# Kernel tuning notes

Measured on AMD Instinct MI355X. Metric: run time of the kernel, lower is better.

The kernel has to match this reference:

```python
import jax, jax.numpy as jnp
import numpy as np

B, IMG_DIM, H, W = 2, 256, 64, 64
PC_C, PC_D = 16, 16          # voxel_dim = PC_C * PC_D = 256
VOXEL_DIM = PC_C * PC_D
QK_DIM = 256                 # out_channels of img_conv / voxel_conv


def _conv1x1(x, w, b):
    # x: [B, Cin, H, W], w: [Cout, Cin], b: [Cout]  (1x1 conv == per-pixel matmul)
    return jnp.einsum('bchw,oc->bohw', x, w) + b[None, :, None, None]


def setup_inputs() -> dict:
    key = jax.random.key(0)
    ks = jax.random.split(key, 10)
    s = 0.02
    return {
        'img': jax.random.normal(ks[0], (B, IMG_DIM, H, W), jnp.float32),
        'pc': jax.random.normal(ks[1], (B, PC_D, H, W, PC_C), jnp.float32),  # dense() layout [B,D,H,W,C]
        'img_conv_w': jax.random.normal(ks[2], (QK_DIM, IMG_DIM), jnp.float32) * s,
        'img_conv_b': jnp.zeros((QK_DIM,), jnp.float32),
        'voxel_conv_w': jax.random.normal(ks[3], (QK_DIM, VOXEL_DIM), jnp.float32) * s,
        'voxel_conv_b': jnp.zeros((QK_DIM,), jnp.float32),
        'img_v_w': jax.random.normal(ks[4], (IMG_DIM, IMG_DIM), jnp.float32) * s,
        'img_v_b': jnp.zeros((IMG_DIM,), jnp.float32),
        'voxel_v_w': jax.random.normal(ks[5], (VOXEL_DIM, VOXEL_DIM), jnp.float32) * s,
        'voxel_v_b': jnp.zeros((VOXEL_DIM,), jnp.float32),
    }


def reference(img, pc, img_conv_w, img_conv_b, voxel_conv_w, voxel_conv_b,
              img_v_w, img_v_b, voxel_v_w, voxel_v_b):
    b, c_img, h, w = img.shape
    # pc.dense() -> permute(0,4,1,2,3) -> [B, C, D, H, W] -> [B, C*D, H, W]
    pc = jnp.transpose(pc, (0, 4, 1, 2, 3))
    pcb, pcc, pcd, pch, pcw = pc.shape
    pc2 = pc.reshape(pcb, pcc * pcd, pch, pcw)
    n = h * w  # == pch * pcw (required by the bmms)

    img_q = _conv1x1(img, img_conv_w, img_conv_b).reshape(b, QK_DIM, n).transpose(0, 2, 1)  # [B, N, 256]
    pc_k = _conv1x1(pc2, voxel_conv_w, voxel_conv_b).reshape(b, QK_DIM, n)                  # [B, 256, N]
    # unscaled single-head cross attention, softmax over voxel positions
    attn = jax.nn.softmax(jnp.einsum('bnc,bcm->bnm', img_q, pc_k), axis=-1)                 # [B, N_img, N_pc]

    img_v = _conv1x1(img, img_v_w, img_v_b).reshape(b, c_img, n)                            # [B, C_img, N]
    img_v = jnp.einsum('bcn,bmn->bcm', img_v, attn).reshape(b, c_img, h, w)                 # img_v @ attn^T

    pc_v = _conv1x1(pc2, voxel_v_w, voxel_v_b).reshape(b, pcc * pcd, n)                     # [B, C*D, N]
    pc_v = jnp.einsum('bcn,bmn->bcm', pc_v, attn).reshape(b, pcc, pcd, pch, pcw)
    return (img_v, pc_v)
```

## Files before the change

### kernel.cpp

```cpp
#include <hip/hip_runtime.h>
#include <hip/hip_bf16.h>


typedef __hip_bfloat16 bf16;
typedef __attribute__((ext_vector_type(8))) short bf16x8;
typedef __attribute__((ext_vector_type(4))) float f32x4;

#define AS1 __attribute__((address_space(1)))
#define AS3 __attribute__((address_space(3)))

__device__ __forceinline__ void gld_lds16(const bf16* g, bf16* s) {
    __builtin_amdgcn_global_load_lds((const AS1 void*)g, (AS3 void*)s, 16, 0, 0);
}

__global__ __launch_bounds__(256) void proj_kernel(
    const float* __restrict__ img, const float* __restrict__ pc,
    const float* __restrict__ Wq,  const float* __restrict__ bq,
    const float* __restrict__ Wk,  const float* __restrict__ bk,
    const float* __restrict__ Wvi, const float* __restrict__ bvi,
    const float* __restrict__ Wvp, const float* __restrict__ bvp,
    bf16* __restrict__ Qw, bf16* __restrict__ Ktw, bf16* __restrict__ Vall)
{
    __shared__ __align__(16) bf16 XT[64][264];
    __shared__ __align__(16) bf16 Wst[256 * 32];

    const int blk = blockIdx.x;
    const int s   = blk >> 8;
    const int b   = (blk >> 7) & 1;
    const int g   = (blk >> 6) & 1;
    const int n0  = (blk & 63) * 64;
    const int tid = threadIdx.x;

    if (s == 0) {
        const float* src = img + b * 1048576;
        for (int k = 0; k < 16; k++) {
            const int i = tid + k * 256;
            const int cin = i >> 4, nl4 = (i & 15) * 4;
            const float4 v = *(const float4*)&src[cin * 4096 + n0 + nl4];
            XT[nl4 + 0][cin] = __float2bfloat16(v.x);
            XT[nl4 + 1][cin] = __float2bfloat16(v.y);
            XT[nl4 + 2][cin] = __float2bfloat16(v.z);
            XT[nl4 + 3][cin] = __float2bfloat16(v.w);
        }
    } else {
        const float* src = pc + b * 1048576;
        for (int k = 0; k < 16; k++) {
            const int d = k, u = tid;
            const int nl = u >> 2, c4 = (u & 3) * 4;
            const float4 v = *(const float4*)&src[d * 65536 + (n0 + nl) * 16 + c4];
            XT[nl][(c4 + 0) * 16 + d] = __float2bfloat16(v.x);
            XT[nl][(c4 + 1) * 16 + d] = __float2bfloat16(v.y);
            XT[nl][(c4 + 2) * 16 + d] = __float2bfloat16(v.z);
            XT[nl][(c4 + 3) * 16 + d] = __float2bfloat16(v.w);
        }
    }

    const float* W = s ? (g ? Wvp : Wk) : (g ? Wvi : Wq);
    const float* Bv = s ? (g ? bvp : bk) : (g ? bvi : bq);

    const int wv = tid >> 6, lane = tid & 63, l16 = lane & 15, quad = lane >> 4;
    const int ob = wv * 64;

    f32x4 acc[4][4] = {};

    for (int ks = 0; ks < 8; ks++) {
        const int k0 = ks * 32;
        __syncthreads();
        for (int j = 0; j < 8; j++) {
            const int idx = j * 256 + tid;
            const int row = idx >> 3, c4 = (idx & 7) * 4;
            const float4 v = *(const float4*)&W[row * 256 + k0 + c4];
            bf16 t4[4];
            t4[0] = __float2bfloat16(v.x); t4[1] = __float2bfloat16(v.y);
            t4[2] = __float2bfloat16(v.z); t4[3] = __float2bfloat16(v.w);
            const int sl = (c4 >> 3) ^ ((row >> 1) & 3);
            *(uint2*)&Wst[row * 32 + sl * 8 + (c4 & 4)] = *(const uint2*)t4;
        }
        __syncthreads();

        bf16x8 af[4], wf[4];
        for (int ti = 0; ti < 4; ti++)
            af[ti] = *(const bf16x8*)&XT[ti * 16 + l16][k0 + quad * 8];
        for (int tj = 0; tj < 4; tj++) {
            const int rw = ob + tj * 16 + l16;
            wf[tj] = *(const bf16x8*)&Wst[rw * 32 + (quad ^ ((rw >> 1) & 3)) * 8];
        }
        for (int ti = 0; ti < 4; ti++)
            for (int tj = 0; tj < 4; tj++)
                acc[ti][tj] = __builtin_amdgcn_mfma_f32_16x16x32_bf16(af[ti], wf[tj], acc[ti][tj], 0, 0, 0);
    }

    if (g == 0) {
        bf16* D1 = (s ? Ktw : Qw) + b * (4096 * 256);
        for (int tj = 0; tj < 4; tj++) {
            const int o = ob + tj * 16 + l16;
            const float bias = Bv[o];
            for (int ti = 0; ti < 4; ti++) {
                const int nl = ti * 16 + quad * 4;
                for (int r = 0; r < 4; r++)
                    D1[(n0 + nl + r) * 256 + o] = __float2bfloat16(acc[ti][tj][r] + bias);
            }
        }
    } else {
        bf16* D2 = Vall + b * (512 * 4096) + (s ? 256 * 4096 : 0);
        for (int tj = 0; tj < 4; tj++) {
            const int o = ob + tj * 16 + l16;
            const float bias = Bv[o];
            for (int ti = 0; ti < 4; ti++) {
                const int nl = ti * 16 + quad * 4;
                bf16 pv[4];
                for (int r = 0; r < 4; r++)
                    pv[r] = __float2bfloat16(acc[ti][tj][r] + bias);
                *(uint2*)&D2[o * 4096 + n0 + nl] = *(const uint2*)pv;
            }
        }
    }
}

__global__ __launch_bounds__(256, 4) void attn_s_kernel(
    const bf16* __restrict__ Qw, const bf16* __restrict__ Ktw,
    bf16* __restrict__ Pt, float* __restrict__ Lpart)
{
    __shared__ __align__(16) bf16 smem[2][8192];

    const int b  = blockIdx.z;
    const int q0 = blockIdx.y * 128;
    const int p0 = blockIdx.x * 128;
    const bf16* Aq = Qw  + b * (4096 * 256);
    const bf16* Ak = Ktw + b * (4096 * 256);

    const int tid = threadIdx.x;
    const int wv = tid >> 6, lane = tid & 63, l16 = lane & 15, quad = lane >> 4;
    const int wr = wv >> 1, wc = wv & 1;

    int aoff[4], boff[4];
    for (int t = 0; t < 4; t++) {
        const int rowa = wr * 64 + t * 16 + l16;
        aoff[t] = rowa * 32 + (quad ^ ((rowa >> 1) & 3)) * 8;
        const int rowb = wc * 64 + t * 16 + l16;
        boff[t] = rowb * 32 + (quad ^ ((rowb >> 1) & 3)) * 8;
    }

    const int arow0 = tid >> 2;
    const int kswz = ((tid & 3) ^ ((arow0 >> 1) & 3)) * 8;
    const bf16* Ag0 = Ak + (p0 + arow0) * 256 + kswz;
    const bf16* Ag1 = Ak + (p0 + 64 + arow0) * 256 + kswz;
    const bf16* Bg0 = Aq + (q0 + arow0) * 256 + kswz;
    const bf16* Bg1 = Aq + (q0 + 64 + arow0) * 256 + kswz;

    f32x4 acc[4][4] = {};

#define SSTAGE(buf, ks)                                                 \
    do {                                                                \
        const int _k = (ks) * 32;                                       \
        bf16* _s = &smem[(buf)][0];                                     \
        gld_lds16(Ag0 + _k, _s + tid * 8);                              \
        gld_lds16(Ag1 + _k, _s + 2048 + tid * 8);                       \
        gld_lds16(Bg0 + _k, _s + 4096 + tid * 8);                       \
        gld_lds16(Bg1 + _k, _s + 6144 + tid * 8);                       \
    } while (0)

    SSTAGE(0, 0);
    int cur = 0;
    for (int ks = 0; ks < 8; ks++) {
        if (ks + 1 < 8) {
            SSTAGE(cur ^ 1, ks + 1);
            asm volatile("s_waitcnt vmcnt(4)" ::: "memory");
        } else {
            asm volatile("s_waitcnt vmcnt(0)" ::: "memory");
        }
        __builtin_amdgcn_s_barrier();
        __builtin_amdgcn_sched_barrier(0);

        const bf16* As_ = &smem[cur][0];
        const bf16* Bs_ = &smem[cur][4096];
        bf16x8 af[4], bfr[4];
        for (int t = 0; t < 4; t++) af[t]  = *(const bf16x8*)&As_[aoff[t]];
        for (int t = 0; t < 4; t++) bfr[t] = *(const bf16x8*)&Bs_[boff[t]];
        __builtin_amdgcn_s_setprio(1);
        for (int ti = 0; ti < 4; ti++)
            for (int tj = 0; tj < 4; tj++)
                acc[ti][tj] = __builtin_amdgcn_mfma_f32_16x16x32_bf16(af[ti], bfr[tj], acc[ti][tj], 0, 0, 0);
        __builtin_amdgcn_s_setprio(0);

        asm volatile("s_waitcnt lgkmcnt(0)" ::: "memory");
        __builtin_amdgcn_s_barrier();
        cur ^= 1;
    }
#undef SSTAGE

    __syncthreads();

    bf16* T = &smem[0][0];
    const int strip = blockIdx.x * 2 + wr;
    for (int tj = 0; tj < 4; tj++) {
        const int ql = wc * 64 + tj * 16 + l16;
        const int sw = (ql & 7) << 3;
        float partial = 0.0f;
        for (int ti = 0; ti < 4; ti++) {
            const int pb = wr * 64 + ti * 16 + quad * 4;
            bf16 pv[4];
            for (int r = 0; r < 4; r++) {
                const float e = __expf(fminf(acc[ti][tj][r], 80.0f));
                partial += e;
                pv[r] = __float2bfloat16(e);
            }
            *(uint2*)&T[ql * 128 + (pb ^ sw)] = *(const uint2*)pv;
        }
        partial += __shfl_xor(partial, 16);
        partial += __shfl_xor(partial, 32);
        if (lane < 16)
            Lpart[(size_t)(b * 4096 + q0 + ql) * 64 + strip] = partial;
    }
    __syncthreads();

    bf16* Ptile = Pt + (size_t)((b * 32 + (q0 >> 7)) * 32 + (p0 >> 7)) * 16384;
    for (int j = 0; j < 8; j++) {
        const int qr = wv * 32 + j * 4 + (lane >> 4);
        const int pcm = (lane & 15) * 8;
        const bf16x8 v = *(const bf16x8*)&T[qr * 128 + (pcm ^ ((qr & 7) << 3))];
        *(bf16x8*)&Ptile[qr * 128 + pcm] = v;
    }
}

__global__ __launch_bounds__(256) void lred_kernel(
    const float* __restrict__ Lpart, float* __restrict__ Linv)
{
    const int row = blockIdx.x * 256 + threadIdx.x;
    const float4* lp = (const float4*)&Lpart[(size_t)row * 64];
    float s = 0.0f;
    for (int i = 0; i < 16; i++) {
        const float4 v = lp[i];
        s += v.x + v.y + v.z + v.w;
    }
    Linv[row] = 1.0f / fmaxf(s, 1e-30f);
}

__global__ __launch_bounds__(512, 2) void attn_o_kernel(
    const bf16* __restrict__ Vall, const bf16* __restrict__ Pt,
    const float* __restrict__ Linv, float* __restrict__ out)
{
    __shared__ __align__(16) bf16 smem[2][4][8192];

    const int orig = blockIdx.x;
    const int L = (orig & 7) * 32 + (orig >> 3);
    const int b   = L >> 7;
    const int rem = L & 127;
    const int c0  = (rem & 3) * 128;
    const int q0  = (rem >> 2) * 128;

    const bf16* A  = Vall + (size_t)b * 512 * 4096;
    const bf16* Bt = Pt + (size_t)((b * 32 + (q0 >> 7)) * 32) * 16384;

    const int tid = threadIdx.x;
    const int grp = tid >> 8;
    const int t8  = tid & 255;
    const int wv = t8 >> 6, lane = t8 & 63, l16 = lane & 15, quad = lane >> 4;
    const int wr = wv >> 1, wc = wv & 1;

    int aoff[4], boff[4];
    for (int t = 0; t < 4; t++) {
        const int rowa = wr * 64 + t * 16 + l16;
        aoff[t] = rowa * 32 + (quad ^ ((rowa >> 1) & 3)) * 8;
        const int rowb = wc * 64 + t * 16 + l16;
        boff[t] = rowb * 32 + (quad ^ ((rowb >> 1) & 3)) * 8;
    }

    const int arow = t8 >> 2;
    const int kswz = ((t8 & 3) ^ ((arow >> 1) & 3)) * 8;
    const bf16* Ag0 = A + (c0 + arow) * 4096 + kswz;
    const bf16* Ag1 = A + (c0 + 64 + arow) * 4096 + kswz;

    f32x4 acc[4][4] = {};

#define STAGE(buf, ks)                                                  \
    do {                                                                \
        const int _kk = grp * 2048 + (ks) * 32;                         \
        bf16* _s = &smem[grp][(buf)][0];                                \
        gld_lds16(Ag0 + _kk, _s + t8 * 8);                              \
        gld_lds16(Ag1 + _kk, _s + 2048 + t8 * 8);                       \
        const bf16* _bp = Bt + (size_t)(_kk >> 7) * 16384               \
                          + arow * 128 + (_kk & 127) + kswz;            \
        gld_lds16(_bp, _s + 4096 + t8 * 8);                             \
        gld_lds16(_bp + 8192, _s + 6144 + t8 * 8);                      \
    } while (0)

    STAGE(0, 0);
    STAGE(1, 1);
    STAGE(2, 2);
    for (int ks = 0; ks < 64; ks++) {
        if (ks + 3 < 64) {
            STAGE((ks + 3) & 3, ks + 3);
            asm volatile("s_waitcnt vmcnt(12)" ::: "memory");
        } else if (ks + 2 < 64) {
            asm volatile("s_waitcnt vmcnt(8)" ::: "memory");
        } else if (ks + 1 < 64) {
            asm volatile("s_waitcnt vmcnt(4)" ::: "memory");
        } else {
            asm volatile("s_waitcnt vmcnt(0)" ::: "memory");
        }
        __builtin_amdgcn_s_barrier();
        __builtin_amdgcn_sched_barrier(0);

        const bf16* As_ = &smem[grp][ks & 3][0];
        const bf16* Bs_ = &smem[grp][ks & 3][4096];
        bf16x8 af[4], bfr[4];
        for (int t = 0; t < 4; t++) af[t]  = *(const bf16x8*)&As_[aoff[t]];
        for (int t = 0; t < 4; t++) bfr[t] = *(const bf16x8*)&Bs_[boff[t]];
        __builtin_amdgcn_s_setprio(1);
        for (int ti = 0; ti < 4; ti++)
            for (int tj = 0; tj < 4; tj++)
                acc[ti][tj] = __builtin_amdgcn_mfma_f32_16x16x32_bf16(af[ti], bfr[tj], acc[ti][tj], 0, 0, 0);
        __builtin_amdgcn_s_setprio(0);

        asm volatile("s_waitcnt lgkmcnt(0)" ::: "memory");
        __builtin_amdgcn_s_barrier();
    }
#undef STAGE

    __syncthreads();

    float* comb = (float*)&smem[0][0][0];
    if (grp == 0) {
        for (int ti = 0; ti < 4; ti++)
            for (int tj = 0; tj < 4; tj++)
                for (int r = 0; r < 4; r++)
                    comb[(wr * 64 + ti * 16 + quad * 4 + r) * 128 + wc * 64 + tj * 16 + l16]
                        = acc[ti][tj][r];
    }
    __syncthreads();
    if (grp == 1) {
        for (int ti = 0; ti < 4; ti++)
            for (int tj = 0; tj < 4; tj++)
                for (int r = 0; r < 4; r++)
                    comb[(wr * 64 + ti * 16 + quad * 4 + r) * 128 + wc * 64 + tj * 16 + l16]
                        += acc[ti][tj][r];
    }
    __syncthreads();

    const int cl = tid >> 2, qb = (tid & 3) * 32;
    const int c_ = c0 + cl;
    const size_t base = (c_ < 256)
        ? ((size_t)b * 1048576 + (size_t)c_ * 4096)
        : (2097152u + (size_t)b * 1048576 + (size_t)(c_ - 256) * 4096);
    for (int j = 0; j < 8; j++) {
        const float4 v = *(const float4*)&comb[cl * 128 + qb + j * 4];
        const float4 l = *(const float4*)&Linv[b * 4096 + q0 + qb + j * 4];
        float4 o;
        o.x = v.x * l.x; o.y = v.y * l.y; o.z = v.z * l.z; o.w = v.w * l.w;
        *(float4*)&out[base + q0 + qb + j * 4] = o;
    }
}

extern "C" void kernel_launch(void* const* d_in, const int* in_sizes, int n_in,
                              void* d_out, int out_size, void* d_ws, size_t ws_size,
                              hipStream_t stream)
{
    const float* img = (const float*)d_in[0];
    const float* pc  = (const float*)d_in[1];
    const float* Wq  = (const float*)d_in[2];
    const float* bq  = (const float*)d_in[3];
    const float* Wk  = (const float*)d_in[4];
    const float* bk  = (const float*)d_in[5];
    const float* Wvi = (const float*)d_in[6];
    const float* bvi = (const float*)d_in[7];
    const float* Wvp = (const float*)d_in[8];
    const float* bvp = (const float*)d_in[9];

    char* ws = (char*)d_ws;
    bf16*  Qw    = (bf16*)(ws);
    bf16*  Ktw   = (bf16*)(ws + (4ull  << 20));
    bf16*  Vall  = (bf16*)(ws + (8ull  << 20));
    bf16*  Pt    = (bf16*)(ws + (16ull << 20));
    float* Lpart = (float*)(ws + (80ull << 20));
    float* Linv  = (float*)(ws + (82ull << 20));

    proj_kernel<<<512, 256, 0, stream>>>(img, pc, Wq, bq, Wk, bk,
                                         Wvi, bvi, Wvp, bvp, Qw, Ktw, Vall);
    attn_s_kernel<<<dim3(32, 32, 2), 256, 0, stream>>>(Qw, Ktw, Pt, Lpart);
    lred_kernel<<<32, 256, 0, stream>>>(Lpart, Linv);
    attn_o_kernel<<<256, 512, 0, stream>>>(Vall, Pt, Linv, (float*)d_out);
}
```

Measured before the change: 182.1 us.

## Pre-tile Q, K, V and P into swizzled 128x32 k-slabs for contiguous LDS loads

The projection kernel now stages its output through shared memory and writes Q, K^T, V and the P tiles into a blocked layout. Each 128-row by 32-k slab is stored contiguously with the LDS XOR swizzle already applied. The attention kernels can then issue fully contiguous 16-byte global-to-LDS loads per stage instead of strided row gathers. This is meant to cut memory transaction overhead and TLB/cache-line waste, at the cost of extra LDS round trips and barriers in the projection epilogue.

Result: slower. 192.4 us (+5.6%).

```diff
diff --git a/kernel.cpp b/kernel.cpp
--- a/kernel.cpp
+++ b/kernel.cpp
@@ -91,27 +91,55 @@
     }
 
     if (g == 0) {
-        bf16* D1 = (s ? Ktw : Qw) + b * (4096 * 256);
+        bf16* Db = (s ? Ktw : Qw) + (size_t)(b * 32 + (n0 >> 7)) * 32768;
+        const int h = (n0 >> 6) & 1;
+        __syncthreads();
         for (int tj = 0; tj < 4; tj++) {
             const int o = ob + tj * 16 + l16;
             const float bias = Bv[o];
             for (int ti = 0; ti < 4; ti++) {
                 const int nl = ti * 16 + quad * 4;
                 for (int r = 0; r < 4; r++)
-                    D1[(n0 + nl + r) * 256 + o] = __float2bfloat16(acc[ti][tj][r] + bias);
+                    XT[nl + r][o] = __float2bfloat16(acc[ti][tj][r] + bias);
             }
         }
+        __syncthreads();
+        const int row = tid >> 2, sl = tid & 3;
+        const int grow = h * 64 + row;
+        const int phys = (sl ^ ((grow >> 1) & 3)) * 8;
+        for (int kt = 0; kt < 8; kt++) {
+            const bf16x8 v = *(const bf16x8*)&XT[row][kt * 32 + sl * 8];
+            *(bf16x8*)&Db[kt * 4096 + grow * 32 + phys] = v;
+        }
     } else {
-        bf16* D2 = Vall + b * (512 * 4096) + (s ? 256 * 4096 : 0);
-        for (int tj = 0; tj < 4; tj++) {
-            const int o = ob + tj * 16 + l16;
-            const float bias = Bv[o];
-            for (int ti = 0; ti < 4; ti++) {
-                const int nl = ti * 16 + quad * 4;
-                bf16 pv[4];
-                for (int r = 0; r < 4; r++)
-                    pv[r] = __float2bfloat16(acc[ti][tj][r] + bias);
-                *(uint2*)&D2[o * 4096 + n0 + nl] = *(const uint2*)pv;
+        bf16* T2 = &XT[0][0];
+        const int kt0 = n0 >> 5;
+        for (int p = 0; p < 2; p++) {
+            __syncthreads();
+            if ((wv >> 1) == p) {
+                for (int tj = 0; tj < 4; tj++) {
+                    const int o = ob + tj * 16 + l16;
+                    const int r_ = o & 127;
+                    const float bias = Bv[o];
+                    for (int ti = 0; ti < 4; ti++) {
+                        const int nl = ti * 16 + quad * 4;
+                        bf16 pv[4];
+                        for (int r = 0; r < 4; r++)
+                            pv[r] = __float2bfloat16(acc[ti][tj][r] + bias);
+                        *(uint2*)&T2[r_ * 72 + nl] = *(const uint2*)pv;
+                    }
+                }
+            }
+            __syncthreads();
+            const int row2 = tid >> 2, sl = tid & 3;
+            for (int kl = 0; kl < 2; kl++) {
+                for (int j3 = 0; j3 < 2; j3++) {
+                    const int row = j3 * 64 + row2;
+                    const int phys = (sl ^ ((row >> 1) & 3)) * 8;
+                    const bf16x8 v = *(const bf16x8*)&T2[row * 72 + kl * 32 + sl * 8];
+                    bf16* Vp = Vall + (size_t)((b * 4 + s * 2 + p) * 128 + kt0 + kl) * 4096;
+                    *(bf16x8*)&Vp[row * 32 + phys] = v;
+                }
             }
         }
     }
@@ -124,10 +152,11 @@
     __shared__ __align__(16) bf16 smem[2][8192];
 
     const int b  = blockIdx.z;
-    const int q0 = blockIdx.y * 128;
-    const int p0 = blockIdx.x * 128;
-    const bf16* Aq = Qw  + b * (4096 * 256);
-    const bf16* Ak = Ktw + b * (4096 * 256);
+    const int qt = blockIdx.y, pt = blockIdx.x;
+    const int q0 = qt * 128;
+
+    const bf16* QP  = Qw  + (size_t)(b * 32 + qt) * 32768 + threadIdx.x * 8;
+    const bf16* KtP = Ktw + (size_t)(b * 32 + pt) * 32768 + threadIdx.x * 8;
 
     const int tid = threadIdx.x;
     const int wv = tid >> 6, lane = tid & 63, l16 = lane & 15, quad = lane >> 4;
@@ -141,23 +170,16 @@
         boff[t] = rowb * 32 + (quad ^ ((rowb >> 1) & 3)) * 8;
     }
 
-    const int arow0 = tid >> 2;
-    const int kswz = ((tid & 3) ^ ((arow0 >> 1) & 3)) * 8;
-    const bf16* Ag0 = Ak + (p0 + arow0) * 256 + kswz;
-    const bf16* Ag1 = Ak + (p0 + 64 + arow0) * 256 + kswz;
-    const bf16* Bg0 = Aq + (q0 + arow0) * 256 + kswz;
-    const bf16* Bg1 = Aq + (q0 + 64 + arow0) * 256 + kswz;
-
     f32x4 acc[4][4] = {};
 
 #define SSTAGE(buf, ks)                                                 \
     do {                                                                \
-        const int _k = (ks) * 32;                                       \
+        const int _k = (ks) * 4096;                                     \
         bf16* _s = &smem[(buf)][0];                                     \
-        gld_lds16(Ag0 + _k, _s + tid * 8);                              \
-        gld_lds16(Ag1 + _k, _s + 2048 + tid * 8);                       \
-        gld_lds16(Bg0 + _k, _s + 4096 + tid * 8);                       \
-        gld_lds16(Bg1 + _k, _s + 6144 + tid * 8);                       \
+        gld_lds16(KtP + _k,        _s + tid * 8);                       \
+        gld_lds16(KtP + _k + 2048, _s + 2048 + tid * 8);                \
+        gld_lds16(QP  + _k,        _s + 4096 + tid * 8);                \
+        gld_lds16(QP  + _k + 2048, _s + 6144 + tid * 8);                \
     } while (0)
 
     SSTAGE(0, 0);
@@ -192,7 +214,7 @@
     __syncthreads();
 
     bf16* T = &smem[0][0];
-    const int strip = blockIdx.x * 2 + wr;
+    const int strip = pt * 2 + wr;
     for (int tj = 0; tj < 4; tj++) {
         const int ql = wc * 64 + tj * 16 + l16;
         const int sw = (ql & 7) << 3;
@@ -214,12 +236,12 @@
     }
     __syncthreads();
 
-    bf16* Ptile = Pt + (size_t)((b * 32 + (q0 >> 7)) * 32 + (p0 >> 7)) * 16384;
+    bf16* Ptile = Pt + (size_t)((b * 32 + qt) * 32 + pt) * 16384;
     for (int j = 0; j < 8; j++) {
-        const int qr = wv * 32 + j * 4 + (lane >> 4);
-        const int pcm = (lane & 15) * 8;
-        const bf16x8 v = *(const bf16x8*)&T[qr * 128 + (pcm ^ ((qr & 7) << 3))];
-        *(bf16x8*)&Ptile[qr * 128 + pcm] = v;
+        const int pk = j >> 1, half = j & 1;
+        const int qr = half * 64 + (tid >> 2), sl = tid & 3;
+        const bf16x8 v = *(const bf16x8*)&T[qr * 128 + ((pk * 32 + sl * 8) ^ ((qr & 7) << 3))];
+        *(bf16x8*)&Ptile[pk * 4096 + qr * 32 + (sl ^ ((qr >> 1) & 3)) * 8] = v;
     }
 }
 
@@ -246,17 +268,19 @@
     const int L = (orig & 7) * 32 + (orig >> 3);
     const int b   = L >> 7;
     const int rem = L & 127;
-    const int c0  = (rem & 3) * 128;
-    const int q0  = (rem >> 2) * 128;
-
-    const bf16* A  = Vall + (size_t)b * 512 * 4096;
-    const bf16* Bt = Pt + (size_t)((b * 32 + (q0 >> 7)) * 32) * 16384;
+    const int ct  = rem & 3;
+    const int qt  = rem >> 2;
+    const int c0  = ct * 128;
+    const int q0  = qt * 128;
 
     const int tid = threadIdx.x;
     const int grp = tid >> 8;
     const int t8  = tid & 255;
     const int wv = t8 >> 6, lane = t8 & 63, l16 = lane & 15, quad = lane >> 4;
     const int wr = wv >> 1, wc = wv & 1;
+
+    const bf16* Abase = Vall + (size_t)(b * 4 + ct) * 524288 + t8 * 8;
+    const bf16* Bbase = Pt   + (size_t)(b * 32 + qt) * 524288 + t8 * 8;
 
     int aoff[4], boff[4];
     for (int t = 0; t < 4; t++) {
@@ -266,23 +290,16 @@
         boff[t] = rowb * 32 + (quad ^ ((rowb >> 1) & 3)) * 8;
     }
 
-    const int arow = t8 >> 2;
-    const int kswz = ((t8 & 3) ^ ((arow >> 1) & 3)) * 8;
-    const bf16* Ag0 = A + (c0 + arow) * 4096 + kswz;
-    const bf16* Ag1 = A + (c0 + 64 + arow) * 4096 + kswz;
-
     f32x4 acc[4][4] = {};
 
 #define STAGE(buf, ks)                                                  \
     do {                                                                \
-        const int _kk = grp * 2048 + (ks) * 32;                         \
+        const int _kt = (grp * 64 + (ks)) * 4096;                       \
         bf16* _s = &smem[grp][(buf)][0];                                \
-        gld_lds16(Ag0 + _kk, _s + t8 * 8);                              \
-        gld_lds16(Ag1 + _kk, _s + 2048 + t8 * 8);                       \
-        const bf16* _bp = Bt + (size_t)(_kk >> 7) * 16384               \
-                          + arow * 128 + (_kk & 127) + kswz;            \
-        gld_lds16(_bp, _s + 4096 + t8 * 8);                             \
-        gld_lds16(_bp + 8192, _s + 6144 + t8 * 8);                      \
+        gld_lds16(Abase + _kt,        _s + t8 * 8);                     \
+        gld_lds16(Abase + _kt + 2048, _s + 2048 + t8 * 8);              \
+        gld_lds16(Bbase + _kt,        _s + 4096 + t8 * 8);              \
+        gld_lds16(Bbase + _kt + 2048, _s + 6144 + t8 * 8);              \
     } while (0)
 
     STAGE(0, 0);
```

## Widen score tile to 256x128 with 512 threads sharing the Q tile

Applied to the files above, without the earlier changes.

The score kernel now has each block compute a 256(pc) by 128(q) tile with 8 waves instead of 128x128 with 4 waves. The Q operand tile is staged once and reused across twice as many K rows, which cuts global and LDS load traffic per output. The transpose buffer switches from an XOR swizzle to a padded stride of 264, and each block writes two P tiles. The trade is more LDS per block and fewer blocks in the grid, which may lower occupancy.

Measured after the change: 186.1 us. +2.2%, slower.

```diff
diff --git a/kernel.cpp b/kernel.cpp
--- a/kernel.cpp
+++ b/kernel.cpp
@@ -117,15 +117,15 @@
     }
 }
 
-__global__ __launch_bounds__(256, 4) void attn_s_kernel(
+__global__ __launch_bounds__(512, 2) void attn_s_kernel(
     const bf16* __restrict__ Qw, const bf16* __restrict__ Ktw,
     bf16* __restrict__ Pt, float* __restrict__ Lpart)
 {
-    __shared__ __align__(16) bf16 smem[2][8192];
+    __shared__ __align__(16) bf16 smem[33792];
 
     const int b  = blockIdx.z;
     const int q0 = blockIdx.y * 128;
-    const int p0 = blockIdx.x * 128;
+    const int p0 = blockIdx.x * 256;
     const bf16* Aq = Qw  + b * (4096 * 256);
     const bf16* Ak = Ktw + b * (4096 * 256);
 
@@ -138,26 +138,24 @@
         const int rowa = wr * 64 + t * 16 + l16;
         aoff[t] = rowa * 32 + (quad ^ ((rowa >> 1) & 3)) * 8;
         const int rowb = wc * 64 + t * 16 + l16;
-        boff[t] = rowb * 32 + (quad ^ ((rowb >> 1) & 3)) * 8;
-    }
-
-    const int arow0 = tid >> 2;
-    const int kswz = ((tid & 3) ^ ((arow0 >> 1) & 3)) * 8;
-    const bf16* Ag0 = Ak + (p0 + arow0) * 256 + kswz;
-    const bf16* Ag1 = Ak + (p0 + 64 + arow0) * 256 + kswz;
-    const bf16* Bg0 = Aq + (q0 + arow0) * 256 + kswz;
-    const bf16* Bg1 = Aq + (q0 + 64 + arow0) * 256 + kswz;
+        boff[t] = 8192 + rowb * 32 + (quad ^ ((rowb >> 1) & 3)) * 8;
+    }
+
+    const int arow = tid >> 2;
+    const int kswz = ((tid & 3) ^ ((arow >> 1) & 3)) * 8;
+    const bf16* Ag0 = Ak + (p0 + arow) * 256 + kswz;
+    const bf16* Ag1 = Ak + (p0 + 128 + arow) * 256 + kswz;
+    const bf16* Bg0 = Aq + (q0 + arow) * 256 + kswz;
 
     f32x4 acc[4][4] = {};
 
 #define SSTAGE(buf, ks)                                                 \
     do {                                                                \
         const int _k = (ks) * 32;                                       \
-        bf16* _s = &smem[(buf)][0];                                     \
+        bf16* _s = &smem[(buf) * 12288];                                \
         gld_lds16(Ag0 + _k, _s + tid * 8);                              \
-        gld_lds16(Ag1 + _k, _s + 2048 + tid * 8);                       \
-        gld_lds16(Bg0 + _k, _s + 4096 + tid * 8);                       \
-        gld_lds16(Bg1 + _k, _s + 6144 + tid * 8);                       \
+        gld_lds16(Ag1 + _k, _s + 4096 + tid * 8);                       \
+        gld_lds16(Bg0 + _k, _s + 8192 + tid * 8);                       \
     } while (0)
 
     SSTAGE(0, 0);
@@ -165,18 +163,17 @@
     for (int ks = 0; ks < 8; ks++) {
         if (ks + 1 < 8) {
             SSTAGE(cur ^ 1, ks + 1);
-            asm volatile("s_waitcnt vmcnt(4)" ::: "memory");
+            asm volatile("s_waitcnt vmcnt(3)" ::: "memory");
         } else {
             asm volatile("s_waitcnt vmcnt(0)" ::: "memory");
         }
         __builtin_amdgcn_s_barrier();
         __builtin_amdgcn_sched_barrier(0);
 
-        const bf16* As_ = &smem[cur][0];
-        const bf16* Bs_ = &smem[cur][4096];
+        const bf16* S_ = &smem[cur * 12288];
         bf16x8 af[4], bfr[4];
-        for (int t = 0; t < 4; t++) af[t]  = *(const bf16x8*)&As_[aoff[t]];
-        for (int t = 0; t < 4; t++) bfr[t] = *(const bf16x8*)&Bs_[boff[t]];
+        for (int t = 0; t < 4; t++) af[t]  = *(const bf16x8*)&S_[aoff[t]];
+        for (int t = 0; t < 4; t++) bfr[t] = *(const bf16x8*)&S_[boff[t]];
         __builtin_amdgcn_s_setprio(1);
         for (int ti = 0; ti < 4; ti++)
             for (int tj = 0; tj < 4; tj++)
@@ -191,11 +188,10 @@
 
     __syncthreads();
 
-    bf16* T = &smem[0][0];
-    const int strip = blockIdx.x * 2 + wr;
+    bf16* T = &smem[0];
+    const int strip = blockIdx.x * 4 + wr;
     for (int tj = 0; tj < 4; tj++) {
         const int ql = wc * 64 + tj * 16 + l16;
-        const int sw = (ql & 7) << 3;
         float partial = 0.0f;
         for (int ti = 0; ti < 4; ti++) {
             const int pb = wr * 64 + ti * 16 + quad * 4;
@@ -205,7 +201,7 @@
                 partial += e;
                 pv[r] = __float2bfloat16(e);
             }
-            *(uint2*)&T[ql * 128 + (pb ^ sw)] = *(const uint2*)pv;
+            *(uint2*)&T[ql * 264 + pb] = *(const uint2*)pv;
         }
         partial += __shfl_xor(partial, 16);
         partial += __shfl_xor(partial, 32);
@@ -214,12 +210,14 @@
     }
     __syncthreads();
 
-    bf16* Ptile = Pt + (size_t)((b * 32 + (q0 >> 7)) * 32 + (p0 >> 7)) * 16384;
-    for (int j = 0; j < 8; j++) {
-        const int qr = wv * 32 + j * 4 + (lane >> 4);
-        const int pcm = (lane & 15) * 8;
-        const bf16x8 v = *(const bf16x8*)&T[qr * 128 + (pcm ^ ((qr & 7) << 3))];
-        *(bf16x8*)&Ptile[qr * 128 + pcm] = v;
+    for (int h = 0; h < 2; h++) {
+        bf16* Ptile = Pt + (size_t)((b * 32 + blockIdx.y) * 32 + blockIdx.x * 2 + h) * 16384;
+        for (int j = 0; j < 4; j++) {
+            const int qr = wv * 16 + j * 4 + (lane >> 4);
+            const int pcm = (lane & 15) * 8;
+            const bf16x8 v = *(const bf16x8*)&T[qr * 264 + h * 128 + pcm];
+            *(bf16x8*)&Ptile[qr * 128 + pcm] = v;
+        }
     }
 }
 
@@ -377,7 +375,7 @@
 
     proj_kernel<<<512, 256, 0, stream>>>(img, pc, Wq, bq, Wk, bk,
                                          Wvi, bvi, Wvp, bvp, Qw, Ktw, Vall);
-    attn_s_kernel<<<dim3(32, 32, 2), 256, 0, stream>>>(Qw, Ktw, Pt, Lpart);
+    attn_s_kernel<<<dim3(16, 32, 2), 512, 0, stream>>>(Qw, Ktw, Pt, Lpart);
     lred_kernel<<<32, 256, 0, stream>>>(Lpart, Linv);
     attn_o_kernel<<<256, 512, 0, stream>>>(Vall, Pt, Linv, (float*)d_out);
 }
```

## Pre-convert projection weights to bf16 and double-buffer them via direct LDS loads

Applied to the files above, without the earlier changes.

Adds a small kernel that converts the four fp32 weight matrices once per call into bf16, pre-swizzled per k-tile. The projection kernel then streams each 256x32 tile into a double-buffered LDS area with global_load_lds, prefetching the next tile while the MFMAs run on the current one. This removes the per-block fp32 loads and conversions, which were repeated by every block, and the two syncthreads per k-step. The cost is one extra kernel launch and twice the LDS for weights, which may reduce occupancy. It also relies on manual waitcnt and barrier handling.

New measurement: 181.6 us. Within noise of the previous version (-0.3%).

```diff
diff --git a/kernel.cpp b/kernel.cpp
--- a/kernel.cpp
+++ b/kernel.cpp
@@ -13,16 +13,39 @@
     __builtin_amdgcn_global_load_lds((const AS1 void*)g, (AS3 void*)s, 16, 0, 0);
 }
 
+__global__ __launch_bounds__(256) void wconv_kernel(
+    const float* __restrict__ Wq, const float* __restrict__ Wvi,
+    const float* __restrict__ Wk, const float* __restrict__ Wvp,
+    bf16* __restrict__ Wbf)
+{
+    const int m  = blockIdx.x >> 3;
+    const int kt = blockIdx.x & 7;
+    const float* W = (m == 0) ? Wq : (m == 1) ? Wvi : (m == 2) ? Wk : Wvp;
+    bf16* D = Wbf + (size_t)(m * 8 + kt) * 8192;
+    const int tid = threadIdx.x;
+    for (int j = 0; j < 4; j++) {
+        const int slot = j * 256 + tid;
+        const int row = slot >> 2, sl = slot & 3;
+        const float4 a = *(const float4*)&W[row * 256 + kt * 32 + sl * 8];
+        const float4 b = *(const float4*)&W[row * 256 + kt * 32 + sl * 8 + 4];
+        bf16 t8[8];
+        t8[0] = __float2bfloat16(a.x); t8[1] = __float2bfloat16(a.y);
+        t8[2] = __float2bfloat16(a.z); t8[3] = __float2bfloat16(a.w);
+        t8[4] = __float2bfloat16(b.x); t8[5] = __float2bfloat16(b.y);
+        t8[6] = __float2bfloat16(b.z); t8[7] = __float2bfloat16(b.w);
+        *(bf16x8*)&D[row * 32 + (sl ^ ((row >> 1) & 3)) * 8] = *(const bf16x8*)t8;
+    }
+}
+
 __global__ __launch_bounds__(256) void proj_kernel(
     const float* __restrict__ img, const float* __restrict__ pc,
-    const float* __restrict__ Wq,  const float* __restrict__ bq,
-    const float* __restrict__ Wk,  const float* __restrict__ bk,
-    const float* __restrict__ Wvi, const float* __restrict__ bvi,
-    const float* __restrict__ Wvp, const float* __restrict__ bvp,
+    const bf16*  __restrict__ Wbf,
+    const float* __restrict__ bq,  const float* __restrict__ bk,
+    const float* __restrict__ bvi, const float* __restrict__ bvp,
     bf16* __restrict__ Qw, bf16* __restrict__ Ktw, bf16* __restrict__ Vall)
 {
     __shared__ __align__(16) bf16 XT[64][264];
-    __shared__ __align__(16) bf16 Wst[256 * 32];
+    __shared__ __align__(16) bf16 Wst[2][8192];
 
     const int blk = blockIdx.x;
     const int s   = blk >> 8;
@@ -54,8 +77,10 @@
             XT[nl][(c4 + 3) * 16 + d] = __float2bfloat16(v.w);
         }
     }
-
-    const float* W = s ? (g ? Wvp : Wk) : (g ? Wvi : Wq);
+    __syncthreads();
+
+    const int widx = s * 2 + g;
+    const bf16* Wp = Wbf + (size_t)widx * 65536 + tid * 8;
     const float* Bv = s ? (g ? bvp : bk) : (g ? bvi : bq);
 
     const int wv = tid >> 6, lane = tid & 63, l16 = lane & 15, quad = lane >> 4;
@@ -63,32 +88,48 @@
 
     f32x4 acc[4][4] = {};
 
+#define WSTAGE(buf, ks)                                                 \
+    do {                                                                \
+        const int _o = (ks) * 8192;                                     \
+        bf16* _s = &Wst[(buf)][0];                                      \
+        gld_lds16(Wp + _o,        _s + tid * 8);                        \
+        gld_lds16(Wp + _o + 2048, _s + 2048 + tid * 8);                 \
+        gld_lds16(Wp + _o + 4096, _s + 4096 + tid * 8);                 \
+        gld_lds16(Wp + _o + 6144, _s + 6144 + tid * 8);                 \
+    } while (0)
+
+    WSTAGE(0, 0);
+    int cur = 0;
     for (int ks = 0; ks < 8; ks++) {
+        if (ks + 1 < 8) {
+            WSTAGE(cur ^ 1, ks + 1);
+            asm volatile("s_waitcnt vmcnt(4)" ::: "memory");
+        } else {
+            asm volatile("s_waitcnt vmcnt(0)" ::: "memory");
+        }
+        __builtin_amdgcn_s_barrier();
+        __builtin_amdgcn_sched_barrier(0);
+
         const int k0 = ks * 32;
-        __syncthreads();
-        for (int j = 0; j < 8; j++) {
-            const int idx = j * 256 + tid;
-            const int row = idx >> 3, c4 = (idx & 7) * 4;
-            const float4 v = *(const float4*)&W[row * 256 + k0 + c4];
-            bf16 t4[4];
-            t4[0] = __float2bfloat16(v.x); t4[1] = __float2bfloat16(v.y);
-            t4[2] = __float2bfloat16(v.z); t4[3] = __float2bfloat16(v.w);
-            const int sl = (c4 >> 3) ^ ((row >> 1) & 3);
-            *(uint2*)&Wst[row * 32 + sl * 8 + (c4 & 4)] = *(const uint2*)t4;
-        }
-        __syncthreads();
-
+        const bf16* Ws_ = &Wst[cur][0];
         bf16x8 af[4], wf[4];
         for (int ti = 0; ti < 4; ti++)
             af[ti] = *(const bf16x8*)&XT[ti * 16 + l16][k0 + quad * 8];
         for (int tj = 0; tj < 4; tj++) {
             const int rw = ob + tj * 16 + l16;
-            wf[tj] = *(const bf16x8*)&Wst[rw * 32 + (quad ^ ((rw >> 1) & 3)) * 8];
-        }
+            wf[tj] = *(const bf16x8*)&Ws_[rw * 32 + (quad ^ ((rw >> 1) & 3)) * 8];
+        }
+        __builtin_amdgcn_s_setprio(1);
         for (int ti = 0; ti < 4; ti++)
             for (int tj = 0; tj < 4; tj++)
                 acc[ti][tj] = __builtin_amdgcn_mfma_f32_16x16x32_bf16(af[ti], wf[tj], acc[ti][tj], 0, 0, 0);
-    }
+        __builtin_amdgcn_s_setprio(0);
+
+        asm volatile("s_waitcnt lgkmcnt(0)" ::: "memory");
+        __builtin_amdgcn_s_barrier();
+        cur ^= 1;
+    }
+#undef WSTAGE
 
     if (g == 0) {
         bf16* D1 = (s ? Ktw : Qw) + b * (4096 * 256);
@@ -374,9 +415,11 @@
     bf16*  Pt    = (bf16*)(ws + (16ull << 20));
     float* Lpart = (float*)(ws + (80ull << 20));
     float* Linv  = (float*)(ws + (82ull << 20));
-
-    proj_kernel<<<512, 256, 0, stream>>>(img, pc, Wq, bq, Wk, bk,
-                                         Wvi, bvi, Wvp, bvp, Qw, Ktw, Vall);
+    bf16*  Wbf   = (bf16*)(ws + (83ull << 20));
+
+    wconv_kernel<<<32, 256, 0, stream>>>(Wq, Wvi, Wk, Wvp, Wbf);
+    proj_kernel<<<512, 256, 0, stream>>>(img, pc, Wbf, bq, bk, bvi, bvp,
+                                         Qw, Ktw, Vall);
     attn_s_kernel<<<dim3(32, 32, 2), 256, 0, stream>>>(Qw, Ktw, Pt, Lpart);
     lred_kernel<<<32, 256, 0, stream>>>(Lpart, Linv);
     attn_o_kernel<<<256, 512, 0, stream>>>(Vall, Pt, Linv, (float*)d_out);
```
